# Kernel optimization log

Measured on AMD Instinct MI355X. Metric: run time of the kernel, lower is better.

## Reference

```python
import jax, jax.numpy as jnp
import numpy as np

D = 32      # bond_dim
N = 784     # 28*28 physical sites
HALF = 392  # single_rank = rank // 2
L = 10      # labels
B = 128     # batch


def setup_inputs() -> dict:
    key = jax.random.key(0)
    k0, k1, k2, k3, k4, k5 = jax.random.split(key, 6)
    # per-site 2-component input features; components sum to 1 so the
    # 392-step transfer-matrix product stays numerically stable in fp32
    u = jax.random.uniform(k0, (B, N), dtype=jnp.float32)
    x = jnp.stack([u, 1.0 - u], axis=-1)  # (B, 784, 2)

    eye = jnp.eye(D, dtype=jnp.float32)[None, :, None, :]  # (1, D, 1, D)
    a0 = jax.random.normal(k1, (D, 2), dtype=jnp.float32) / np.float32(np.sqrt(D))
    cores_left = eye + 0.01 * jax.random.normal(k2, (HALF - 1, D, 2, D), dtype=jnp.float32)
    core_mid = 0.05 * jax.random.normal(k3, (D, L, D), dtype=jnp.float32)
    cores_right = eye + 0.01 * jax.random.normal(k4, (HALF - 1, D, 2, D), dtype=jnp.float32)
    a_end = jax.random.normal(k5, (D, 2), dtype=jnp.float32) / np.float32(np.sqrt(D))
    return {"x": x, "a0": a0, "cores_left": cores_left, "core_mid": core_mid,
            "cores_right": cores_right, "a_end": a_end}


def reference(x, a0, cores_left, core_mid, cores_right, a_end):
    # ---- left half: nodes 0..391 contracted with inputs 0..391 ----
    v0 = jnp.einsum('dp,bp->bd', a0, x[:, 0])                       # (B, D)
    # input-contracted transfer matrices for nodes 1..391
    Ml = jnp.einsum('nlpr,bnp->nblr', cores_left, x[:, 1:HALF])      # (391, B, D, D)

    def step_left(c, M):
        return jnp.einsum('bl,blr->br', c, M), None

    left, _ = jax.lax.scan(step_left, v0, Ml)                        # (B, D)

    # ---- right half: nodes 393..784 contracted with inputs 392..783 ----
    r0 = jnp.einsum('dp,bp->bd', a_end, x[:, N - 1])                 # (B, D)
    Mr = jnp.einsum('nlpr,bnp->nblr', cores_right, x[:, HALF:N - 1])  # (391, B, D, D)

    def step_right(c, M):
        return jnp.einsum('blr,br->bl', M, c), None

    right, _ = jax.lax.scan(step_right, r0, Mr, reverse=True)        # (B, D)

    # ---- middle label node: original does einsum('a,aba,a->b') (diagonal!) ----
    mid_diag = jnp.einsum('aba->ab', core_mid)                       # (D, L)
    return jnp.einsum('ba,ba,ac->bc', left, right, mid_diag)         # (B, 10)
```

## Files before the change

### kernel.cpp

```cpp
#include <hip/hip_runtime.h>

#define NSTEP 391
#define NB 128
#define NGRP 16

typedef __attribute__((ext_vector_type(8))) short s8v;
typedef __attribute__((ext_vector_type(16))) float f32x16;

typedef const __attribute__((address_space(1))) void* gas_ptr;
typedef __attribute__((address_space(3))) void* las_ptr;

union I4S8 { int4 i; s8v v; };
union W4S8 { int w[4]; s8v v; };

#define WAITVM(N) do { asm volatile("s_waitcnt vmcnt(" #N ")" ::: "memory"); \
                       __builtin_amdgcn_sched_barrier(0); } while (0)
#define LGKM0     do { asm volatile("s_waitcnt lgkmcnt(0)" ::: "memory");   \
                       __builtin_amdgcn_sched_barrier(0); } while (0)

__device__ __forceinline__ int pack_hi(float a, float b) {
    return (__float_as_int(b) & 0xffff0000) | ((unsigned)__float_as_int(a) >> 16);
}
__device__ __forceinline__ float trunc_bf(float a) {
    return __int_as_float(__float_as_int(a) & 0xffff0000);
}
__device__ __forceinline__ int cvtpk(float a, float b) {
    int r;
    asm("v_cvt_pk_bf16_f32 %0, %1, %2" : "=v"(r) : "v"(a), "v"(b));
    return r;
}

__global__ __launch_bounds__(256) void prep(
    const float* __restrict__ coresL, const float* __restrict__ coresR,
    int* __restrict__ aprep) {
    const int bid = blockIdx.x;
    const int side = bid >= NSTEP;
    const int t = bid - side * NSTEP;
    const float* st = (side ? coresR : coresL) + t * 2048;
    int* out = aprep + (size_t)(side * NSTEP + t) * 2048;
    for (int o = threadIdx.x; o < 2048; o += 256) {
        const int f = o >> 8, lane = (o >> 2) & 63, w = o & 3;
        const int part = f >> 2, p = (f >> 1) & 1, j = f & 1;
        const int h = lane >> 5, c = lane & 31;
        const int k0 = j * 16 + h * 8 + w * 2;
        float e0, e1;
        if (!side) { e0 = st[c * 64 + p * 32 + k0];  e1 = st[c * 64 + p * 32 + k0 + 1]; }
        else       { e0 = st[k0 * 64 + p * 32 + c];  e1 = st[(k0 + 1) * 64 + p * 32 + c]; }
        out[o] = (part == 0) ? pack_hi(e0, e1)
                             : pack_hi(e0 - trunc_bf(e0), e1 - trunc_bf(e1));
    }
}

__device__ __forceinline__ void bpack(const float* d, bool h0, W4S8& b1h, W4S8& b2h,
                                      W4S8& b1l, W4S8& b2l) {
#if __has_builtin(__builtin_amdgcn_permlane32_swap)
    int hw[8], lw[8];
    #pragma unroll
    for (int q = 0; q < 8; ++q) {
        float e = d[2 * q], o = d[2 * q + 1];
        hw[q] = __builtin_amdgcn_perm(__float_as_uint(o), __float_as_uint(e), 0x07060302u);
        lw[q] = cvtpk(e - trunc_bf(e), o - trunc_bf(o));
    }
    {
        auto r0 = __builtin_amdgcn_permlane32_swap(hw[0], hw[2], false, false);
        b1h.w[0] = r0[0]; b1h.w[2] = r0[1];
        auto r1 = __builtin_amdgcn_permlane32_swap(hw[1], hw[3], false, false);
        b1h.w[1] = r1[0]; b1h.w[3] = r1[1];
        auto r2 = __builtin_amdgcn_permlane32_swap(hw[4], hw[6], false, false);
        b2h.w[0] = r2[0]; b2h.w[2] = r2[1];
        auto r3 = __builtin_amdgcn_permlane32_swap(hw[5], hw[7], false, false);
        b2h.w[1] = r3[0]; b2h.w[3] = r3[1];
        auto r4 = __builtin_amdgcn_permlane32_swap(lw[0], lw[2], false, false);
        b1l.w[0] = r4[0]; b1l.w[2] = r4[1];
        auto r5 = __builtin_amdgcn_permlane32_swap(lw[1], lw[3], false, false);
        b1l.w[1] = r5[0]; b1l.w[3] = r5[1];
        auto r6 = __builtin_amdgcn_permlane32_swap(lw[4], lw[6], false, false);
        b2l.w[0] = r6[0]; b2l.w[2] = r6[1];
        auto r7 = __builtin_amdgcn_permlane32_swap(lw[5], lw[7], false, false);
        b2l.w[1] = r7[0]; b2l.w[3] = r7[1];
    }
    (void)h0;
#else
    float sx[16];
    #pragma unroll
    for (int r = 0; r < 16; ++r) sx[r] = __shfl_xor(d[r], 32);
    float B1[8], B2[8];
    #pragma unroll
    for (int m = 0; m < 4; ++m) {
        B1[m]     = h0 ? d[m]      : sx[4 + m];
        B1[4 + m] = h0 ? sx[m]     : d[4 + m];
        B2[m]     = h0 ? d[8 + m]  : sx[12 + m];
        B2[4 + m] = h0 ? sx[8 + m] : d[12 + m];
    }
    #pragma unroll
    for (int ww = 0; ww < 4; ++ww) {
        b1h.w[ww] = pack_hi(B1[2 * ww], B1[2 * ww + 1]);
        b2h.w[ww] = pack_hi(B2[2 * ww], B2[2 * ww + 1]);
        b1l.w[ww] = cvtpk(B1[2 * ww] - trunc_bf(B1[2 * ww]),
                          B1[2 * ww + 1] - trunc_bf(B1[2 * ww + 1]));
        b2l.w[ww] = cvtpk(B2[2 * ww] - trunc_bf(B2[2 * ww]),
                          B2[2 * ww + 1] - trunc_bf(B2[2 * ww + 1]));
    }
#endif
}

__device__ __forceinline__ void mstep(float* d, const I4S8* fr,
                                      const W4S8& b1h, const W4S8& b2h,
                                      const W4S8& b1l, const W4S8& b2l, float2 xv) {
    f32x16 acc0 = {}; f32x16 acc1 = {};
    acc0 = __builtin_amdgcn_mfma_f32_32x32x16_bf16(fr[0].v, b1h.v, acc0, 0, 0, 0);
    acc1 = __builtin_amdgcn_mfma_f32_32x32x16_bf16(fr[2].v, b1h.v, acc1, 0, 0, 0);
    acc0 = __builtin_amdgcn_mfma_f32_32x32x16_bf16(fr[1].v, b2h.v, acc0, 0, 0, 0);
    acc1 = __builtin_amdgcn_mfma_f32_32x32x16_bf16(fr[3].v, b2h.v, acc1, 0, 0, 0);
    acc0 = __builtin_amdgcn_mfma_f32_32x32x16_bf16(fr[0].v, b1l.v, acc0, 0, 0, 0);
    acc1 = __builtin_amdgcn_mfma_f32_32x32x16_bf16(fr[2].v, b1l.v, acc1, 0, 0, 0);
    acc0 = __builtin_amdgcn_mfma_f32_32x32x16_bf16(fr[1].v, b2l.v, acc0, 0, 0, 0);
    acc1 = __builtin_amdgcn_mfma_f32_32x32x16_bf16(fr[3].v, b2l.v, acc1, 0, 0, 0);
    acc0 = __builtin_amdgcn_mfma_f32_32x32x16_bf16(fr[4].v, b1h.v, acc0, 0, 0, 0);
    acc1 = __builtin_amdgcn_mfma_f32_32x32x16_bf16(fr[6].v, b1h.v, acc1, 0, 0, 0);
    acc0 = __builtin_amdgcn_mfma_f32_32x32x16_bf16(fr[5].v, b2h.v, acc0, 0, 0, 0);
    acc1 = __builtin_amdgcn_mfma_f32_32x32x16_bf16(fr[7].v, b2h.v, acc1, 0, 0, 0);
    #pragma unroll
    for (int r = 0; r < 16; ++r) d[r] = fmaf(xv.y, acc1[r], xv.x * acc0[r]);
}

__device__ __forceinline__ void issue_tile(const int* tb, int* slot, int lane) {
    #pragma unroll
    for (int f = 0; f < 8; ++f)
        __builtin_amdgcn_global_load_lds((gas_ptr)(tb + f * 256 + lane * 4),
                                         (las_ptr)(slot + f * 256), 16, 0, 0);
}

__global__ __launch_bounds__(256) void stage1(
    const float* __restrict__ x, const int* __restrict__ aprep,
    float* __restrict__ qws) {
    __shared__ int ring[4][2][2048];
    __shared__ float2 xls[4][2][28];
    const int wv = threadIdx.x >> 6;
    const int w = blockIdx.x * 4 + wv;
    const int lane = threadIdx.x & 63;
    const int side = w >> 10;
    const int g = (w >> 6) & 15;
    const int bp = w & 63;
    const int a = g * 24 + (g < 7 ? g : 7);
    const int len = 24 + (g < 7 ? 1 : 0);
    const int h = lane >> 5, col = lane & 31;
    const bool h0 = (h == 0);

    const float2* xA = (const float2*)x + (bp * 2) * 784;
    const float2* xB = (const float2*)x + (bp * 2 + 1) * 784;
    if (lane < len) {
        int t = side ? (392 + a + lane) : (a + len - lane);
        xls[wv][0][lane] = xA[t];
        xls[wv][1][lane] = xB[t];
    }

    float d0[16], d1[16];
    #pragma unroll
    for (int r = 0; r < 16; ++r) {
        float iv = (((r & 3) + 8 * (r >> 2) + 4 * h) == col) ? 1.0f : 0.0f;
        d0[r] = iv; d1[r] = iv;
    }

    const int* tbase = aprep + (size_t)side * NSTEP * 2048;
    auto taddr = [&](int j) {
        int t = side ? (a + j) : (a + len - 1 - j);
        t = t < 0 ? 0 : (t > 390 ? 390 : t);
        return tbase + (size_t)t * 2048;
    };

    issue_tile(taddr(0), ring[wv][0], lane);
    issue_tile(taddr(1), ring[wv][1], lane);

    for (int j = 0; j < len; ++j) {
        int* slot = ring[wv][j & 1];
        W4S8 p1h, p2h, p1l, p2l, q1h, q2h, q1l, q2l;
        bpack(d0, h0, p1h, p2h, p1l, p2l);
        bpack(d1, h0, q1h, q2h, q1l, q2l);
        WAITVM(8);
        I4S8 fr[8];
        #pragma unroll
        for (int f = 0; f < 8; ++f)
            fr[f].i = *(const int4*)(slot + f * 256 + lane * 4);
        mstep(d0, fr, p1h, p2h, p1l, p2l, xls[wv][0][j]);
        mstep(d1, fr, q1h, q2h, q1l, q2l, xls[wv][1][j]);
        LGKM0;
        issue_tile(taddr(j + 2), slot, lane);
    }
    WAITVM(0);

    float4* q0 = (float4*)(qws + (size_t)(side * 2048 + (bp * 2) * 16 + g) * 1024 + lane * 16);
    float4* q1 = (float4*)(qws + (size_t)(side * 2048 + (bp * 2 + 1) * 16 + g) * 1024 + lane * 16);
    q0[0] = make_float4(d0[0], d0[1], d0[2], d0[3]);
    q0[1] = make_float4(d0[4], d0[5], d0[6], d0[7]);
    q0[2] = make_float4(d0[8], d0[9], d0[10], d0[11]);
    q0[3] = make_float4(d0[12], d0[13], d0[14], d0[15]);
    q1[0] = make_float4(d1[0], d1[1], d1[2], d1[3]);
    q1[1] = make_float4(d1[4], d1[5], d1[6], d1[7]);
    q1[2] = make_float4(d1[8], d1[9], d1[10], d1[11]);
    q1[3] = make_float4(d1[12], d1[13], d1[14], d1[15]);
}

__global__ __launch_bounds__(64) void stage2(
    const float* __restrict__ x, const float* __restrict__ a0,
    const float* __restrict__ aend, const float* __restrict__ qws,
    float* __restrict__ lw, float* __restrict__ rw) {
    const int b = blockIdx.x >> 1, side = blockIdx.x & 1;
    const int lane = threadIdx.x;
    const int j = lane >> 5, c = lane & 31;
    const float2* xb = (const float2*)x + b * 784;
    float v;
    if (side == 0) { float2 x0 = xb[0];   v = fmaf(a0[c * 2], x0.x, a0[c * 2 + 1] * x0.y); }
    else           { float2 xe = xb[783]; v = fmaf(aend[c * 2], xe.x, aend[c * 2 + 1] * xe.y); }
    for (int i = 0; i < NGRP; ++i) {
        const int g = side ? (NGRP - 1 - i) : i;
        const int task = side * 2048 + b * 16 + g;
        const float4* qp = (const float4*)(qws + (size_t)task * 1024 + (j * 32 + c) * 16);
        float q[16];
        #pragma unroll
        for (int u = 0; u < 4; ++u) {
            float4 t4 = qp[u];
            q[4 * u] = t4.x; q[4 * u + 1] = t4.y; q[4 * u + 2] = t4.z; q[4 * u + 3] = t4.w;
        }
        float s0 = 0.f, s1 = 0.f, s2 = 0.f, s3 = 0.f;
        #pragma unroll
        for (int r = 0; r < 16; r += 4) {
            s0 = fmaf(__shfl(v, 0 + 8 * (r >> 2) + 4 * j, 64), q[r + 0], s0);
            s1 = fmaf(__shfl(v, 1 + 8 * (r >> 2) + 4 * j, 64), q[r + 1], s1);
            s2 = fmaf(__shfl(v, 2 + 8 * (r >> 2) + 4 * j, 64), q[r + 2], s2);
            s3 = fmaf(__shfl(v, 3 + 8 * (r >> 2) + 4 * j, 64), q[r + 3], s3);
        }
        float s = (s0 + s1) + (s2 + s3);
        s += __shfl_xor(s, 32);
        v = s;
    }
    if (lane < 32) { (side ? rw : lw)[b * 32 + c] = v; }
}

__global__ __launch_bounds__(64) void mps_final(
    const float* __restrict__ lw, const float* __restrict__ rw,
    const float* __restrict__ mid,
    float* __restrict__ out) {
    const int b = blockIdx.x;
    const int a = threadIdx.x & 31;
    float pa = lw[b * 32 + a] * rw[b * 32 + a];
    #pragma unroll
    for (int c = 0; c < 10; ++c) {
        float s = pa * mid[a * 320 + c * 32 + a];
        s += __shfl_xor(s, 16, 32);
        s += __shfl_xor(s, 8, 32);
        s += __shfl_xor(s, 4, 32);
        s += __shfl_xor(s, 2, 32);
        s += __shfl_xor(s, 1, 32);
        if (threadIdx.x == 0) out[b * 10 + c] = s;
    }
}

extern "C" void kernel_launch(void* const* d_in, const int* in_sizes, int n_in,
                              void* d_out, int out_size, void* d_ws, size_t ws_size,
                              hipStream_t stream) {
    const float* x      = (const float*)d_in[0];
    const float* a0     = (const float*)d_in[1];
    const float* coresL = (const float*)d_in[2];
    const float* mid    = (const float*)d_in[3];
    const float* coresR = (const float*)d_in[4];
    const float* aend   = (const float*)d_in[5];

    int*   aprep = (int*)d_ws;
    float* qws   = (float*)d_ws + 2 * NSTEP * 2048;
    float* lw    = qws + 4096 * 1024;
    float* rw    = lw + NB * 32;
    float* out   = (float*)d_out;

    prep<<<dim3(2 * NSTEP), dim3(256), 0, stream>>>(coresL, coresR, aprep);
    stage1<<<dim3(512), dim3(256), 0, stream>>>(x, aprep, qws);
    stage2<<<dim3(2 * NB), dim3(64), 0, stream>>>(x, a0, aend, qws, lw, rw);
    mps_final<<<dim3(NB), dim3(64), 0, stream>>>(lw, rw, mid, out);
}
```

Baseline: 72.61 us.

## Share transfer-matrix tiles across a block's waves and remap blocks per XCD

```diff
diff --git a/kernel.cpp b/kernel.cpp
--- a/kernel.cpp
+++ b/kernel.cpp
@@ -16,6 +16,8 @@
 #define WAITVM(N) do { asm volatile("s_waitcnt vmcnt(" #N ")" ::: "memory"); \
                        __builtin_amdgcn_sched_barrier(0); } while (0)
 #define LGKM0     do { asm volatile("s_waitcnt lgkmcnt(0)" ::: "memory");   \
+                       __builtin_amdgcn_sched_barrier(0); } while (0)
+#define SBAR      do { __builtin_amdgcn_s_barrier();                        \
                        __builtin_amdgcn_sched_barrier(0); } while (0)
 
 __device__ __forceinline__ int pack_hi(float a, float b) {
@@ -124,43 +126,44 @@
     for (int r = 0; r < 16; ++r) d[r] = fmaf(xv.y, acc1[r], xv.x * acc0[r]);
 }
 
-__device__ __forceinline__ void issue_tile(const int* tb, int* slot, int lane) {
-    #pragma unroll
-    for (int f = 0; f < 8; ++f)
-        __builtin_amdgcn_global_load_lds((gas_ptr)(tb + f * 256 + lane * 4),
-                                         (las_ptr)(slot + f * 256), 16, 0, 0);
-}
-
-__global__ __launch_bounds__(256) void stage1(
+__device__ __forceinline__ void issue_part(const int* tb, int* slot, int lane, int wv) {
+    const int f0 = wv * 2;
+    __builtin_amdgcn_global_load_lds((gas_ptr)(tb + f0 * 256 + lane * 4),
+                                     (las_ptr)(slot + f0 * 256), 16, 0, 0);
+    __builtin_amdgcn_global_load_lds((gas_ptr)(tb + (f0 + 1) * 256 + lane * 4),
+                                     (las_ptr)(slot + (f0 + 1) * 256), 16, 0, 0);
+}
+
+__global__ __launch_bounds__(256, 4) void stage1(
     const float* __restrict__ x, const int* __restrict__ aprep,
     float* __restrict__ qws) {
-    __shared__ int ring[4][2][2048];
-    __shared__ float2 xls[4][2][28];
+    __shared__ int ring[2][2048];
+    __shared__ float2 xls[4][28];
     const int wv = threadIdx.x >> 6;
-    const int w = blockIdx.x * 4 + wv;
     const int lane = threadIdx.x & 63;
-    const int side = w >> 10;
-    const int g = (w >> 6) & 15;
-    const int bp = w & 63;
+    const int dsp = blockIdx.x;
+    const int xcd = dsp & 7;
+    const int s = dsp >> 3;
+    const int stream = xcd + 8 * (s & 3);
+    const int inb = s >> 2;
+    const int side = stream >> 4;
+    const int g = stream & 15;
+    const int b = inb * 4 + wv;
     const int a = g * 24 + (g < 7 ? g : 7);
     const int len = 24 + (g < 7 ? 1 : 0);
     const int h = lane >> 5, col = lane & 31;
     const bool h0 = (h == 0);
 
-    const float2* xA = (const float2*)x + (bp * 2) * 784;
-    const float2* xB = (const float2*)x + (bp * 2 + 1) * 784;
+    const float2* xb2 = (const float2*)x + b * 784;
     if (lane < len) {
         int t = side ? (392 + a + lane) : (a + len - lane);
-        xls[wv][0][lane] = xA[t];
-        xls[wv][1][lane] = xB[t];
-    }
-
-    float d0[16], d1[16];
-    #pragma unroll
-    for (int r = 0; r < 16; ++r) {
-        float iv = (((r & 3) + 8 * (r >> 2) + 4 * h) == col) ? 1.0f : 0.0f;
-        d0[r] = iv; d1[r] = iv;
-    }
+        xls[wv][lane] = xb2[t];
+    }
+
+    float d0[16];
+    #pragma unroll
+    for (int r = 0; r < 16; ++r)
+        d0[r] = (((r & 3) + 8 * (r >> 2) + 4 * h) == col) ? 1.0f : 0.0f;
 
     const int* tbase = aprep + (size_t)side * NSTEP * 2048;
     auto taddr = [&](int j) {
@@ -169,36 +172,31 @@
         return tbase + (size_t)t * 2048;
     };
 
-    issue_tile(taddr(0), ring[wv][0], lane);
-    issue_tile(taddr(1), ring[wv][1], lane);
+    issue_part(taddr(0), ring[0], lane, wv);
+    issue_part(taddr(1), ring[1], lane, wv);
 
     for (int j = 0; j < len; ++j) {
-        int* slot = ring[wv][j & 1];
-        W4S8 p1h, p2h, p1l, p2l, q1h, q2h, q1l, q2l;
-        bpack(d0, h0, p1h, p2h, p1l, p2l);
-        bpack(d1, h0, q1h, q2h, q1l, q2l);
-        WAITVM(8);
+        int* slot = ring[j & 1];
+        W4S8 b1h, b2h, b1l, b2l;
+        bpack(d0, h0, b1h, b2h, b1l, b2l);
+        WAITVM(2);
+        SBAR;
         I4S8 fr[8];
         #pragma unroll
         for (int f = 0; f < 8; ++f)
             fr[f].i = *(const int4*)(slot + f * 256 + lane * 4);
-        mstep(d0, fr, p1h, p2h, p1l, p2l, xls[wv][0][j]);
-        mstep(d1, fr, q1h, q2h, q1l, q2l, xls[wv][1][j]);
+        mstep(d0, fr, b1h, b2h, b1l, b2l, xls[wv][j]);
         LGKM0;
-        issue_tile(taddr(j + 2), slot, lane);
+        SBAR;
+        issue_part(taddr(j + 2), slot, lane, wv);
     }
     WAITVM(0);
 
-    float4* q0 = (float4*)(qws + (size_t)(side * 2048 + (bp * 2) * 16 + g) * 1024 + lane * 16);
-    float4* q1 = (float4*)(qws + (size_t)(side * 2048 + (bp * 2 + 1) * 16 + g) * 1024 + lane * 16);
+    float4* q0 = (float4*)(qws + (size_t)(side * 2048 + b * 16 + g) * 1024 + lane * 16);
     q0[0] = make_float4(d0[0], d0[1], d0[2], d0[3]);
     q0[1] = make_float4(d0[4], d0[5], d0[6], d0[7]);
     q0[2] = make_float4(d0[8], d0[9], d0[10], d0[11]);
     q0[3] = make_float4(d0[12], d0[13], d0[14], d0[15]);
-    q1[0] = make_float4(d1[0], d1[1], d1[2], d1[3]);
-    q1[1] = make_float4(d1[4], d1[5], d1[6], d1[7]);
-    q1[2] = make_float4(d1[8], d1[9], d1[10], d1[11]);
-    q1[3] = make_float4(d1[12], d1[13], d1[14], d1[15]);
 }
 
 __global__ __launch_bounds__(64) void stage2(
@@ -273,7 +271,7 @@
     float* out   = (float*)d_out;
 
     prep<<<dim3(2 * NSTEP), dim3(256), 0, stream>>>(coresL, coresR, aprep);
-    stage1<<<dim3(512), dim3(256), 0, stream>>>(x, aprep, qws);
+    stage1<<<dim3(1024), dim3(256), 0, stream>>>(x, aprep, qws);
     stage2<<<dim3(2 * NB), dim3(64), 0, stream>>>(x, a0, aend, qws, lw, rw);
     mps_final<<<dim3(NB), dim3(64), 0, stream>>>(lw, rw, mid, out);
 }
```

New measurement: 67.26 us. 7.4% less time.
